# Kernel optimization log

Measured on AMD Instinct MI355X. Metric: run time of the kernel, lower is better.

Reference implementation:

```python
import jax, jax.numpy as jnp
import numpy as np
from jax import lax

D_MODEL = 128   # n_channels
OUT_C   = 128   # out_channels
D_STATE = 16
EXPAND  = 2
D_INNER = EXPAND * D_MODEL  # 256
D_CONV  = 4
DT_RANK = (D_MODEL + 15) // 16  # 8
LN_EPS  = 1e-5


def setup_inputs() -> dict:
    key = jax.random.key(0)
    ks = jax.random.split(key, 8)
    s = lambda k, shape: jax.random.normal(k, shape, jnp.float32) * 0.02
    return {
        "x1": jax.random.normal(ks[0], (2, D_MODEL, 64, 64), jnp.float32),
        "W_in": s(ks[1], (D_MODEL, 2 * D_INNER)),              # in_proj (no bias)
        "conv_w": s(ks[2], (D_INNER, 1, D_CONV)),              # depthwise conv kernel (O, I/g, K)
        "conv_b": jnp.zeros((D_INNER,), jnp.float32),
        "W_x": s(ks[3], (D_INNER, DT_RANK + 2 * D_STATE)),     # x_proj (no bias)
        "W_dt": s(ks[4], (DT_RANK, D_INNER)),                  # dt_proj
        "b_dt": s(ks[5], (D_INNER,)),
        "A_log": jnp.log(jnp.broadcast_to(
            jnp.arange(1, D_STATE + 1, dtype=jnp.float32), (D_INNER, D_STATE))),
        "D": jnp.ones((D_INNER,), jnp.float32),
        "W_out": s(ks[6], (D_INNER, OUT_C)),                   # out_proj (no bias)
        "ln_g": jnp.ones((OUT_C,), jnp.float32),
        "ln_b": jnp.zeros((OUT_C,), jnp.float32),
    }


def _mamba(x, W_in, conv_w, conv_b, W_x, W_dt, b_dt, A_log, D, W_out):
    # x: (b, L, d_model)
    b, L, _ = x.shape
    xz = x @ W_in                               # (b, L, 2*d_inner)
    xin, z = jnp.split(xz, 2, axis=-1)
    # causal depthwise conv1d over L
    xp = jnp.pad(xin, ((0, 0), (D_CONV - 1, 0), (0, 0)))
    xc = lax.conv_general_dilated(
        xp, conv_w, window_strides=(1,), padding='VALID',
        dimension_numbers=('NLC', 'OIL', 'NLC'),
        feature_group_count=D_INNER)
    xc = jax.nn.silu(xc + conv_b)               # (b, L, d_inner)
    # input-dependent SSM params
    xdbl = xc @ W_x                             # (b, L, dt_rank + 2*d_state)
    dt, Bm, Cm = jnp.split(xdbl, [DT_RANK, DT_RANK + D_STATE], axis=-1)
    dt = jax.nn.softplus(dt @ W_dt + b_dt)      # (b, L, d_inner)
    A = -jnp.exp(A_log)                         # (d_inner, d_state)
    dA = jnp.exp(dt[..., None] * A)                             # (b, L, d_inner, d_state)
    dBu = dt[..., None] * Bm[:, :, None, :] * xc[..., None]     # (b, L, d_inner, d_state)

    def step(h, inp):
        dA_t, dBu_t, C_t = inp                  # (b,d,s), (b,d,s), (b,s)
        h = dA_t * h + dBu_t
        y = jnp.einsum('bds,bs->bd', h, C_t)
        return h, y

    h0 = jnp.zeros((b, D_INNER, D_STATE), xc.dtype)
    _, ys = lax.scan(step, h0, (dA.transpose(1, 0, 2, 3),
                                dBu.transpose(1, 0, 2, 3),
                                Cm.transpose(1, 0, 2)))
    y = ys.transpose(1, 0, 2) + xc * D          # (b, L, d_inner)
    y = y * jax.nn.silu(z)                      # gated
    return y @ W_out                            # (b, L, out_c)


def reference(x1, W_in, conv_w, conv_b, W_x, W_dt, b_dt, A_log, D, W_out, ln_g, ln_b):
    b, c, h, w = x1.shape
    x = x1.transpose(0, 2, 3, 1).reshape(b, h * w, c)
    y = _mamba(x, W_in, conv_w, conv_b, W_x, W_dt, b_dt, A_log, D, W_out)
    mu = y.mean(-1, keepdims=True)
    var = ((y - mu) ** 2).mean(-1, keepdims=True)
    y = (y - mu) * lax.rsqrt(var + LN_EPS) * ln_g + ln_b
    return y.reshape(b, h, w, OUT_C).transpose(0, 3, 1, 2)
```

## Files before the change

### kernel.cpp

```cpp
#include <hip/hip_runtime.h>
#include <math.h>

#define B_ 2
#define DMODEL 128
#define DIN 256
#define DSTATE 16
#define DTR 8
#define OUTC 128
#define Lseq 4096
#define NC 256
#define LC 16

__device__ __forceinline__ float siluf(float x){ return x / (1.f + __expf(-x)); }

__device__ __forceinline__ void build_dA(float e1, float* dAv){
    float e2 = e1*e1, e4 = e2*e2, e8 = e4*e4;
    dAv[0]=e1;         dAv[1]=e2;         dAv[2]=e2*e1;       dAv[3]=e4;
    dAv[4]=e4*e1;      dAv[5]=e4*e2;      dAv[6]=e4*dAv[2];   dAv[7]=e8;
    dAv[8]=e8*e1;      dAv[9]=e8*e2;      dAv[10]=e8*dAv[2];  dAv[11]=e8*e4;
    dAv[12]=e8*dAv[4]; dAv[13]=e8*dAv[5]; dAv[14]=e8*dAv[6];  dAv[15]=e8*e8;
}

__device__ __forceinline__ float softplusf(float a){
    return (a > 20.f) ? a : __logf(1.f + __expf(a));
}

__global__ __launch_bounds__(256) void k_inconv_scan1(const float* __restrict__ x1,
        const float* __restrict__ Win,
        const float* __restrict__ convw, const float* __restrict__ convb,
        const float* __restrict__ Wx, const float* __restrict__ Wdt,
        const float* __restrict__ bdt, const float* __restrict__ Alog,
        float* __restrict__ zs, float* __restrict__ xc, float* __restrict__ dt,
        float* __restrict__ Bm, float* __restrict__ Cm, float2* __restrict__ PSw){
    __shared__ float xt[128*20];
    __shared__ float xcs[16*257];
    __shared__ float xdbl[16*40];
    int blk = blockIdx.x;
    int b  = blk >> 8;
    int cb = blk & 255;
    int l0 = cb << 4;
    int t  = threadIdx.x;

    const float* xb = x1 + (size_t)b * DMODEL * Lseq;
    for (int e = t; e < 128*19; e += 256){
        int c = e / 19, p = e - c*19;
        int l = l0 - 3 + p;
        xt[c*20 + p] = (l >= 0) ? xb[(size_t)c*Lseq + l] : 0.f;
    }
    __syncthreads();

    float acc0[19], acc1[16];
    #pragma unroll
    for (int p=0;p<19;++p) acc0[p]=0.f;
    #pragma unroll
    for (int p=0;p<16;++p) acc1[p]=0.f;
    for (int k=0;k<DMODEL;++k){
        float w0 = Win[k*512 + t];
        float w1 = Win[k*512 + t + 256];
        float xv[19];
        #pragma unroll
        for (int p=0;p<19;++p) xv[p] = xt[k*20 + p];
        #pragma unroll
        for (int p=0;p<19;++p) acc0[p] = fmaf(xv[p], w0, acc0[p]);
        #pragma unroll
        for (int p=0;p<16;++p) acc1[p] = fmaf(xv[p+3], w1, acc1[p]);
    }
    {
        float* zp = zs + ((size_t)(b*Lseq + l0))*DIN + t;
        #pragma unroll
        for (int p=0;p<16;++p) zp[p*DIN] = siluf(acc1[p]);
    }

    {
        float cw0 = convw[t*4+0], cw1 = convw[t*4+1], cw2 = convw[t*4+2], cw3 = convw[t*4+3];
        float bb = convb[t];
        float* xcg = xc + ((size_t)(b*Lseq + l0))*DIN + t;
        #pragma unroll
        for (int l = 0; l < 16; ++l){
            float acc = bb;
            acc = fmaf(acc0[l],   cw0, acc);
            acc = fmaf(acc0[l+1], cw1, acc);
            acc = fmaf(acc0[l+2], cw2, acc);
            acc = fmaf(acc0[l+3], cw3, acc);
            float v = siluf(acc);
            xcs[l*257 + t] = v;
            xcg[l*DIN] = v;
        }
    }
    __syncthreads();

    if (t < 128){
        int jg = t & 7;
        int lg = t >> 3;
        int j0 = jg * 5;
        float a0=0.f, a1=0.f, a2=0.f, a3=0.f, a4=0.f;
        const float* xrow = xcs + lg*257;
        const float* wbase = Wx + j0;
        #pragma unroll 8
        for (int d = 0; d < 256; ++d){
            float xv = xrow[d];
            const float* wr = wbase + d*40;
            a0 = fmaf(xv, wr[0], a0);
            a1 = fmaf(xv, wr[1], a1);
            a2 = fmaf(xv, wr[2], a2);
            a3 = fmaf(xv, wr[3], a3);
            a4 = fmaf(xv, wr[4], a4);
        }
        float* xo = xdbl + lg*40 + j0;
        xo[0]=a0; xo[1]=a1; xo[2]=a2; xo[3]=a3; xo[4]=a4;
    }
    __syncthreads();

    {
        float wd[DTR];
        #pragma unroll
        for (int r=0;r<DTR;++r) wd[r] = Wdt[r*DIN + t];
        float bv = bdt[t];
        float Av[16];
        {
            const float4* Ap = (const float4*)(Alog + t*DSTATE);
            #pragma unroll
            for (int q=0;q<4;++q){
                float4 a = Ap[q];
                Av[q*4]   = -__expf(a.x);
                Av[q*4+1] = -__expf(a.y);
                Av[q*4+2] = -__expf(a.z);
                Av[q*4+3] = -__expf(a.w);
            }
        }
        bool fastA = true;
        #pragma unroll
        for (int i=1;i<16;++i)
            fastA = fastA && (fabsf(Av[i] - (float)(i+1)*Av[0]) <= 1e-6f*fabsf(Av[i]));
        float P[16], S[16];
        #pragma unroll
        for (int s=0;s<16;++s){ P[s]=1.f; S[s]=0.f; }
        float* dtg = dt + ((size_t)(b*Lseq + l0))*DIN + t;
        #pragma unroll 4
        for (int l=0;l<16;++l){
            float a = bv;
            #pragma unroll
            for (int r=0;r<DTR;++r) a = fmaf(xdbl[l*40 + r], wd[r], a);
            float dtv = softplusf(a);
            dtg[l*DIN] = dtv;
            float xcv = xcs[l*257 + t];
            float dx  = dtv*xcv;
            const float4* Bv = (const float4*)&xdbl[l*40 + DTR];
            float4 B0 = Bv[0], B1 = Bv[1], B2 = Bv[2], B3 = Bv[3];
            float dAv[16];
            if (fastA){
                build_dA(__expf(dtv*Av[0]), dAv);
            } else {
                #pragma unroll
                for (int i=0;i<16;++i) dAv[i] = __expf(dtv*Av[i]);
            }
            #define ST1(i, bval) { P[i] *= dAv[i]; S[i] = fmaf(dAv[i], S[i], dx*(bval)); }
            ST1(0,B0.x) ST1(1,B0.y) ST1(2,B0.z) ST1(3,B0.w)
            ST1(4,B1.x) ST1(5,B1.y) ST1(6,B1.z) ST1(7,B1.w)
            ST1(8,B2.x) ST1(9,B2.y) ST1(10,B2.z) ST1(11,B2.w)
            ST1(12,B3.x) ST1(13,B3.y) ST1(14,B3.z) ST1(15,B3.w)
            #undef ST1
        }
        float2* ps = PSw + ((size_t)(b*NC + cb))*4096 + t*DSTATE;
        #pragma unroll
        for (int s=0;s<16;++s) ps[s] = make_float2(P[s], S[s]);
    }
    for (int o = t; o < 512; o += 256){
        int l = o >> 5, q = o & 31;
        float v = xdbl[l*40 + DTR + q];
        size_t g = ((size_t)(b*Lseq + l0 + l))*DSTATE;
        if (q < DSTATE) Bm[g + q] = v;
        else            Cm[g + (q - DSTATE)] = v;
    }
}

__global__ __launch_bounds__(256) void k_scan2(const float2* __restrict__ PSw,
        float* __restrict__ Iw){
    __shared__ float2 gps[16][16];
    __shared__ float  ge [16][16];
    int blk = blockIdx.x;
    int b  = blk >> 8;
    int r0 = (blk & 255) * 16;
    int t  = threadIdx.x;
    int rr = t & 15;
    int cg = t >> 4;
    size_t base = ((size_t)(b*NC + cg*16))*4096 + r0 + rr;
    float Pl[16], Sl[16];
    float Pa = 1.f, Sa = 0.f;
    #pragma unroll
    for (int i=0;i<16;++i){
        float2 ps = PSw[base + (size_t)i*4096];
        Pl[i] = ps.x; Sl[i] = ps.y;
        Pa = ps.x * Pa;
        Sa = fmaf(ps.x, Sa, ps.y);
    }
    gps[cg][rr] = make_float2(Pa, Sa);
    __syncthreads();
    if (t < 16){
        float H = 0.f;
        #pragma unroll
        for (int g=0; g<16; ++g){
            float2 ps = gps[g][t];
            ge[g][t] = H;
            H = fmaf(ps.x, H, ps.y);
        }
    }
    __syncthreads();
    float H = ge[cg][rr];
    #pragma unroll
    for (int i=0;i<16;++i){
        Iw[base + (size_t)i*4096] = H;
        H = fmaf(Pl[i], H, Sl[i]);
    }
}

__global__ __launch_bounds__(256) void k_scan3out(const float* __restrict__ dt,
        const float* __restrict__ xc, const float* __restrict__ zs,
        const float* __restrict__ Bm, const float* __restrict__ Cm,
        const float* __restrict__ Alog, const float* __restrict__ Dv,
        const float* __restrict__ Iw,
        const float* __restrict__ Wout, const float* __restrict__ lng,
        const float* __restrict__ lnb, float* __restrict__ out){
    __shared__ float ysm[256*18];
    __shared__ float os[128*18];
    __shared__ float Bs[LC*DSTATE];
    __shared__ float Cs[LC*DSTATE];
    int blk = blockIdx.x;
    int b = blk >> 8, c = blk & 255;
    int l0 = c * LC;
    int t = threadIdx.x;
    size_t gb = (size_t)(b*Lseq + l0);
    Bs[t] = Bm[gb*DSTATE + t];
    Cs[t] = Cm[gb*DSTATE + t];
    float Av[16];
    {
        const float4* Ap = (const float4*)(Alog + t*DSTATE);
        #pragma unroll
        for (int q=0;q<4;++q){
            float4 a = Ap[q];
            Av[q*4]   = -__expf(a.x);
            Av[q*4+1] = -__expf(a.y);
            Av[q*4+2] = -__expf(a.z);
            Av[q*4+3] = -__expf(a.w);
        }
    }
    bool fastA = true;
    #pragma unroll
    for (int i=1;i<16;++i)
        fastA = fastA && (fabsf(Av[i] - (float)(i+1)*Av[0]) <= 1e-6f*fabsf(Av[i]));
    float h[16];
    {
        const float4* Ip = (const float4*)(Iw + ((size_t)(b*NC + c))*4096 + t*DSTATE);
        #pragma unroll
        for (int q=0;q<4;++q){
            float4 v = Ip[q];
            h[q*4]=v.x; h[q*4+1]=v.y; h[q*4+2]=v.z; h[q*4+3]=v.w;
        }
    }
    float Dd = Dv[t];
    float dtv[LC], xcv[LC], zvv[LC];
    {
        const float* dtp = dt + gb*DIN + t;
        const float* xcp = xc + gb*DIN + t;
        const float* zsp = zs + gb*DIN + t;
        #pragma unroll
        for (int l=0;l<LC;++l){
            dtv[l] = dtp[l*DIN];
            xcv[l] = xcp[l*DIN];
            zvv[l] = zsp[l*DIN];
        }
    }
    __syncthreads();
    #pragma unroll
    for (int l=0;l<LC;++l){
        float dtl = dtv[l];
        float dx  = dtl*xcv[l];
        const float4* Bv = (const float4*)&Bs[l*DSTATE];
        const float4* Cv = (const float4*)&Cs[l*DSTATE];
        float4 B0 = Bv[0], B1 = Bv[1], B2 = Bv[2], B3 = Bv[3];
        float4 C0 = Cv[0], C1 = Cv[1], C2 = Cv[2], C3 = Cv[3];
        float dAv[16];
        if (fastA){
            build_dA(__expf(dtl*Av[0]), dAv);
        } else {
            #pragma unroll
            for (int i=0;i<16;++i) dAv[i] = __expf(dtl*Av[i]);
        }
        float y = 0.f;
        #define ST3(i, bval, cval) { h[i] = fmaf(dAv[i], h[i], dx*(bval)); y = fmaf(h[i], (cval), y); }
        ST3(0,B0.x,C0.x) ST3(1,B0.y,C0.y) ST3(2,B0.z,C0.z) ST3(3,B0.w,C0.w)
        ST3(4,B1.x,C1.x) ST3(5,B1.y,C1.y) ST3(6,B1.z,C1.z) ST3(7,B1.w,C1.w)
        ST3(8,B2.x,C2.x) ST3(9,B2.y,C2.y) ST3(10,B2.z,C2.z) ST3(11,B2.w,C2.w)
        ST3(12,B3.x,C3.x) ST3(13,B3.y,C3.y) ST3(14,B3.z,C3.z) ST3(15,B3.w,C3.w)
        #undef ST3
        ysm[t*18 + l] = (y + Dd*xcv[l])*zvv[l];
    }
    __syncthreads();
    int lg = t >> 5, cg = t & 31;
    int l0t = lg*2, c0 = cg*4;
    float acc[2][4];
    #pragma unroll
    for (int i=0;i<2;++i)
        #pragma unroll
        for (int j=0;j<4;++j) acc[i][j]=0.f;
    #pragma unroll 4
    for (int k=0;k<DIN;++k){
        float2 yv = *(const float2*)&ysm[k*18 + l0t];
        float4 wv = *(const float4*)&Wout[k*OUTC + c0];
        acc[0][0]=fmaf(yv.x,wv.x,acc[0][0]); acc[0][1]=fmaf(yv.x,wv.y,acc[0][1]);
        acc[0][2]=fmaf(yv.x,wv.z,acc[0][2]); acc[0][3]=fmaf(yv.x,wv.w,acc[0][3]);
        acc[1][0]=fmaf(yv.y,wv.x,acc[1][0]); acc[1][1]=fmaf(yv.y,wv.y,acc[1][1]);
        acc[1][2]=fmaf(yv.y,wv.z,acc[1][2]); acc[1][3]=fmaf(yv.y,wv.w,acc[1][3]);
    }
    float4 gm = *(const float4*)&lng[c0];
    float4 bt = *(const float4*)&lnb[c0];
    #pragma unroll
    for (int i=0;i<2;++i){
        float rs = acc[i][0]+acc[i][1]+acc[i][2]+acc[i][3];
        #pragma unroll
        for (int m=16;m>0;m>>=1) rs += __shfl_xor(rs, m, 64);
        float mu = rs * (1.f/128.f);
        float d0 = acc[i][0]-mu, d1 = acc[i][1]-mu, d2 = acc[i][2]-mu, d3 = acc[i][3]-mu;
        float sq = d0*d0+d1*d1+d2*d2+d3*d3;
        #pragma unroll
        for (int m=16;m>0;m>>=1) sq += __shfl_xor(sq, m, 64);
        float rstd = rsqrtf(sq * (1.f/128.f) + 1e-5f);
        int lidx = l0t + i;
        os[(c0+0)*18 + lidx] = d0*rstd*gm.x + bt.x;
        os[(c0+1)*18 + lidx] = d1*rstd*gm.y + bt.y;
        os[(c0+2)*18 + lidx] = d2*rstd*gm.z + bt.z;
        os[(c0+3)*18 + lidx] = d3*rstd*gm.w + bt.w;
    }
    __syncthreads();
    {
        int cc = t >> 1, sel = t & 1;
        const float* ip = &os[cc*18 + sel*8];
        float2 a0 = *(const float2*)(ip);
        float2 a1 = *(const float2*)(ip+2);
        float2 a2 = *(const float2*)(ip+4);
        float2 a3 = *(const float2*)(ip+6);
        float* op = out + ((size_t)(b*OUTC + cc))*Lseq + l0 + sel*8;
        *(float4*)(op)   = make_float4(a0.x,a0.y,a1.x,a1.y);
        *(float4*)(op+4) = make_float4(a2.x,a2.y,a3.x,a3.y);
    }
}

extern "C" void kernel_launch(void* const* d_in, const int* in_sizes, int n_in,
                              void* d_out, int out_size, void* d_ws, size_t ws_size,
                              hipStream_t stream) {
    const float* x1    = (const float*)d_in[0];
    const float* Win   = (const float*)d_in[1];
    const float* convw = (const float*)d_in[2];
    const float* convb = (const float*)d_in[3];
    const float* Wx    = (const float*)d_in[4];
    const float* Wdt   = (const float*)d_in[5];
    const float* bdt   = (const float*)d_in[6];
    const float* Alog  = (const float*)d_in[7];
    const float* Dv    = (const float*)d_in[8];
    const float* Wout  = (const float*)d_in[9];
    const float* lng   = (const float*)d_in[10];
    const float* lnb   = (const float*)d_in[11];
    float* out = (float*)d_out;

    float* ws  = (float*)d_ws;
    float* Iw  = ws;
    float* zs  = Iw  + 2097152;
    float* xc  = zs  + 2097152;
    float* dt  = xc  + 2097152;
    float* Bm  = dt  + 2097152;
    float* Cm  = Bm  + 131072;
    float2* PSw = (float2*)(Cm + 131072);

    k_inconv_scan1<<<512, 256, 0, stream>>>(x1, Win, convw, convb, Wx, Wdt, bdt, Alog,
                                            zs, xc, dt, Bm, Cm, PSw);
    k_scan2       <<<512, 256, 0, stream>>>(PSw, Iw);
    k_scan3out    <<<512, 256, 0, stream>>>(dt, xc, zs, Bm, Cm, Alog, Dv, Iw,
                                            Wout, lng, lnb, out);
}
```

Before: 167.6 us.

## Double block size to 512 threads and split projection work across thread halves

Both the input-projection/scan1 kernel and the scan3/out-projection kernel now launch 512 threads per block instead of 256. In the first kernel, the in_proj GEMM is split so one half computes the xin/conv branch and the other half computes the z gate. The x tile is now loaded as float4 into a padded tile, and the x_proj work is spread over 320 threads. In the output kernel, the out_proj GEMM and LayerNorm now handle one row per thread group instead of two, which raises parallelism and lowers per-thread register pressure. The cost is that half the threads sit idle during the scan phases, and the larger blocks may reduce how many blocks fit on a compute unit at once.

Result: slower. 197.4 us (+17.8%).

```diff
diff --git a/kernel.cpp b/kernel.cpp
--- a/kernel.cpp
+++ b/kernel.cpp
@@ -25,14 +25,14 @@
     return (a > 20.f) ? a : __logf(1.f + __expf(a));
 }
 
-__global__ __launch_bounds__(256) void k_inconv_scan1(const float* __restrict__ x1,
+__global__ __launch_bounds__(512) void k_inconv_scan1(const float* __restrict__ x1,
         const float* __restrict__ Win,
         const float* __restrict__ convw, const float* __restrict__ convb,
         const float* __restrict__ Wx, const float* __restrict__ Wdt,
         const float* __restrict__ bdt, const float* __restrict__ Alog,
         float* __restrict__ zs, float* __restrict__ xc, float* __restrict__ dt,
         float* __restrict__ Bm, float* __restrict__ Cm, float2* __restrict__ PSw){
-    __shared__ float xt[128*20];
+    __shared__ float xt[128*24];
     __shared__ float xcs[16*257];
     __shared__ float xdbl[16*40];
     int blk = blockIdx.x;
@@ -42,36 +42,37 @@
     int t  = threadIdx.x;
 
     const float* xb = x1 + (size_t)b * DMODEL * Lseq;
-    for (int e = t; e < 128*19; e += 256){
-        int c = e / 19, p = e - c*19;
-        int l = l0 - 3 + p;
-        xt[c*20 + p] = (l >= 0) ? xb[(size_t)c*Lseq + l] : 0.f;
-    }
-    __syncthreads();
-
-    float acc0[19], acc1[16];
-    #pragma unroll
-    for (int p=0;p<19;++p) acc0[p]=0.f;
-    #pragma unroll
-    for (int p=0;p<16;++p) acc1[p]=0.f;
-    for (int k=0;k<DMODEL;++k){
-        float w0 = Win[k*512 + t];
-        float w1 = Win[k*512 + t + 256];
-        float xv[19];
-        #pragma unroll
-        for (int p=0;p<19;++p) xv[p] = xt[k*20 + p];
-        #pragma unroll
-        for (int p=0;p<19;++p) acc0[p] = fmaf(xv[p], w0, acc0[p]);
-        #pragma unroll
-        for (int p=0;p<16;++p) acc1[p] = fmaf(xv[p+3], w1, acc1[p]);
-    }
     {
-        float* zp = zs + ((size_t)(b*Lseq + l0))*DIN + t;
-        #pragma unroll
-        for (int p=0;p<16;++p) zp[p*DIN] = siluf(acc1[p]);
-    }
-
-    {
+        float4 z4 = make_float4(0.f,0.f,0.f,0.f);
+        for (int e = t; e < 128*6; e += 512){
+            int c = e / 6, i = e - c*6;
+            int l = l0 - 8 + i*4;
+            float4 v = (l >= 0) ? *(const float4*)&xb[(size_t)c*Lseq + l] : z4;
+            *(float4*)&xt[e*4] = v;
+        }
+    }
+    __syncthreads();
+
+    if (t < 256){
+        float acc0[19];
+        #pragma unroll
+        for (int p=0;p<19;++p) acc0[p]=0.f;
+        #pragma unroll 4
+        for (int k=0;k<128;++k){
+            float w = Win[k*512 + t];
+            const float4* xp = (const float4*)&xt[k*24 + 4];
+            float4 x0=xp[0], x1_=xp[1], x2_=xp[2], x3_=xp[3], x4_=xp[4];
+            acc0[0] =fmaf(x0.y, w, acc0[0]);  acc0[1] =fmaf(x0.z, w, acc0[1]);
+            acc0[2] =fmaf(x0.w, w, acc0[2]);  acc0[3] =fmaf(x1_.x,w, acc0[3]);
+            acc0[4] =fmaf(x1_.y,w, acc0[4]);  acc0[5] =fmaf(x1_.z,w, acc0[5]);
+            acc0[6] =fmaf(x1_.w,w, acc0[6]);  acc0[7] =fmaf(x2_.x,w, acc0[7]);
+            acc0[8] =fmaf(x2_.y,w, acc0[8]);  acc0[9] =fmaf(x2_.z,w, acc0[9]);
+            acc0[10]=fmaf(x2_.w,w, acc0[10]); acc0[11]=fmaf(x3_.x,w, acc0[11]);
+            acc0[12]=fmaf(x3_.y,w, acc0[12]); acc0[13]=fmaf(x3_.z,w, acc0[13]);
+            acc0[14]=fmaf(x3_.w,w, acc0[14]); acc0[15]=fmaf(x4_.x,w, acc0[15]);
+            acc0[16]=fmaf(x4_.y,w, acc0[16]); acc0[17]=fmaf(x4_.z,w, acc0[17]);
+            acc0[18]=fmaf(x4_.w,w, acc0[18]);
+        }
         float cw0 = convw[t*4+0], cw1 = convw[t*4+1], cw2 = convw[t*4+2], cw3 = convw[t*4+3];
         float bb = convb[t];
         float* xcg = xc + ((size_t)(b*Lseq + l0))*DIN + t;
@@ -86,32 +87,49 @@
             xcs[l*257 + t] = v;
             xcg[l*DIN] = v;
         }
-    }
-    __syncthreads();
-
-    if (t < 128){
-        int jg = t & 7;
-        int lg = t >> 3;
-        int j0 = jg * 5;
-        float a0=0.f, a1=0.f, a2=0.f, a3=0.f, a4=0.f;
-        const float* xrow = xcs + lg*257;
-        const float* wbase = Wx + j0;
+    } else {
+        float acc1[16];
+        #pragma unroll
+        for (int p=0;p<16;++p) acc1[p]=0.f;
+        #pragma unroll 4
+        for (int k=0;k<128;++k){
+            float w = Win[k*512 + t];
+            const float4* yp = (const float4*)&xt[k*24 + 8];
+            float4 y0=yp[0], y1=yp[1], y2=yp[2], y3=yp[3];
+            acc1[0] =fmaf(y0.x, w, acc1[0]);  acc1[1] =fmaf(y0.y, w, acc1[1]);
+            acc1[2] =fmaf(y0.z, w, acc1[2]);  acc1[3] =fmaf(y0.w, w, acc1[3]);
+            acc1[4] =fmaf(y1.x, w, acc1[4]);  acc1[5] =fmaf(y1.y, w, acc1[5]);
+            acc1[6] =fmaf(y1.z, w, acc1[6]);  acc1[7] =fmaf(y1.w, w, acc1[7]);
+            acc1[8] =fmaf(y2.x, w, acc1[8]);  acc1[9] =fmaf(y2.y, w, acc1[9]);
+            acc1[10]=fmaf(y2.z, w, acc1[10]); acc1[11]=fmaf(y2.w, w, acc1[11]);
+            acc1[12]=fmaf(y3.x, w, acc1[12]); acc1[13]=fmaf(y3.y, w, acc1[13]);
+            acc1[14]=fmaf(y3.z, w, acc1[14]); acc1[15]=fmaf(y3.w, w, acc1[15]);
+        }
+        float* zp = zs + ((size_t)(b*Lseq + l0))*DIN + (t - 256);
+        #pragma unroll
+        for (int p=0;p<16;++p) zp[p*DIN] = siluf(acc1[p]);
+    }
+    __syncthreads();
+
+    if (t < 320){
+        int row = t / 20;
+        int jg  = t - row*20;
+        int j0  = jg * 2;
+        float a0=0.f, a1=0.f;
+        const float* xrow = xcs + row*257;
+        const float* wb = Wx + j0;
         #pragma unroll 8
         for (int d = 0; d < 256; ++d){
             float xv = xrow[d];
-            const float* wr = wbase + d*40;
-            a0 = fmaf(xv, wr[0], a0);
-            a1 = fmaf(xv, wr[1], a1);
-            a2 = fmaf(xv, wr[2], a2);
-            a3 = fmaf(xv, wr[3], a3);
-            a4 = fmaf(xv, wr[4], a4);
-        }
-        float* xo = xdbl + lg*40 + j0;
-        xo[0]=a0; xo[1]=a1; xo[2]=a2; xo[3]=a3; xo[4]=a4;
-    }
-    __syncthreads();
-
-    {
+            float2 wv = *(const float2*)&wb[d*40];
+            a0 = fmaf(xv, wv.x, a0);
+            a1 = fmaf(xv, wv.y, a1);
+        }
+        *(float2*)&xdbl[row*40 + j0] = make_float2(a0, a1);
+    }
+    __syncthreads();
+
+    if (t < 256){
         float wd[DTR];
         #pragma unroll
         for (int r=0;r<DTR;++r) wd[r] = Wdt[r*DIN + t];
@@ -165,8 +183,8 @@
         #pragma unroll
         for (int s=0;s<16;++s) ps[s] = make_float2(P[s], S[s]);
     }
-    for (int o = t; o < 512; o += 256){
-        int l = o >> 5, q = o & 31;
+    {
+        int l = t >> 5, q = t & 31;
         float v = xdbl[l*40 + DTR + q];
         size_t g = ((size_t)(b*Lseq + l0 + l))*DSTATE;
         if (q < DSTATE) Bm[g + q] = v;
@@ -214,7 +232,7 @@
     }
 }
 
-__global__ __launch_bounds__(256) void k_scan3out(const float* __restrict__ dt,
+__global__ __launch_bounds__(512) void k_scan3out(const float* __restrict__ dt,
         const float* __restrict__ xc, const float* __restrict__ zs,
         const float* __restrict__ Bm, const float* __restrict__ Cm,
         const float* __restrict__ Alog, const float* __restrict__ Dv,
@@ -230,10 +248,13 @@
     int l0 = c * LC;
     int t = threadIdx.x;
     size_t gb = (size_t)(b*Lseq + l0);
-    Bs[t] = Bm[gb*DSTATE + t];
-    Cs[t] = Cm[gb*DSTATE + t];
-    float Av[16];
-    {
+    if (t < 256) Bs[t]       = Bm[gb*DSTATE + t];
+    else         Cs[t - 256] = Cm[gb*DSTATE + (t - 256)];
+
+    float Av[16], h[16], dtv[LC], xcv[LC], zvv[LC];
+    float Dd = 0.f;
+    bool fastA = true;
+    if (t < 256){
         const float4* Ap = (const float4*)(Alog + t*DSTATE);
         #pragma unroll
         for (int q=0;q<4;++q){
@@ -243,23 +264,16 @@
             Av[q*4+2] = -__expf(a.z);
             Av[q*4+3] = -__expf(a.w);
         }
-    }
-    bool fastA = true;
-    #pragma unroll
-    for (int i=1;i<16;++i)
-        fastA = fastA && (fabsf(Av[i] - (float)(i+1)*Av[0]) <= 1e-6f*fabsf(Av[i]));
-    float h[16];
-    {
+        #pragma unroll
+        for (int i=1;i<16;++i)
+            fastA = fastA && (fabsf(Av[i] - (float)(i+1)*Av[0]) <= 1e-6f*fabsf(Av[i]));
         const float4* Ip = (const float4*)(Iw + ((size_t)(b*NC + c))*4096 + t*DSTATE);
         #pragma unroll
         for (int q=0;q<4;++q){
             float4 v = Ip[q];
             h[q*4]=v.x; h[q*4+1]=v.y; h[q*4+2]=v.z; h[q*4+3]=v.w;
         }
-    }
-    float Dd = Dv[t];
-    float dtv[LC], xcv[LC], zvv[LC];
-    {
+        Dd = Dv[t];
         const float* dtp = dt + gb*DIN + t;
         const float* xcp = xc + gb*DIN + t;
         const float* zsp = zs + gb*DIN + t;
@@ -271,77 +285,70 @@
         }
     }
     __syncthreads();
-    #pragma unroll
-    for (int l=0;l<LC;++l){
-        float dtl = dtv[l];
-        float dx  = dtl*xcv[l];
-        const float4* Bv = (const float4*)&Bs[l*DSTATE];
-        const float4* Cv = (const float4*)&Cs[l*DSTATE];
-        float4 B0 = Bv[0], B1 = Bv[1], B2 = Bv[2], B3 = Bv[3];
-        float4 C0 = Cv[0], C1 = Cv[1], C2 = Cv[2], C3 = Cv[3];
-        float dAv[16];
-        if (fastA){
-            build_dA(__expf(dtl*Av[0]), dAv);
-        } else {
-            #pragma unroll
-            for (int i=0;i<16;++i) dAv[i] = __expf(dtl*Av[i]);
-        }
-        float y = 0.f;
-        #define ST3(i, bval, cval) { h[i] = fmaf(dAv[i], h[i], dx*(bval)); y = fmaf(h[i], (cval), y); }
-        ST3(0,B0.x,C0.x) ST3(1,B0.y,C0.y) ST3(2,B0.z,C0.z) ST3(3,B0.w,C0.w)
-        ST3(4,B1.x,C1.x) ST3(5,B1.y,C1.y) ST3(6,B1.z,C1.z) ST3(7,B1.w,C1.w)
-        ST3(8,B2.x,C2.x) ST3(9,B2.y,C2.y) ST3(10,B2.z,C2.z) ST3(11,B2.w,C2.w)
-        ST3(12,B3.x,C3.x) ST3(13,B3.y,C3.y) ST3(14,B3.z,C3.z) ST3(15,B3.w,C3.w)
-        #undef ST3
-        ysm[t*18 + l] = (y + Dd*xcv[l])*zvv[l];
+    if (t < 256){
+        #pragma unroll
+        for (int l=0;l<LC;++l){
+            float dtl = dtv[l];
+            float dx  = dtl*xcv[l];
+            const float4* Bv = (const float4*)&Bs[l*DSTATE];
+            const float4* Cv = (const float4*)&Cs[l*DSTATE];
+            float4 B0 = Bv[0], B1 = Bv[1], B2 = Bv[2], B3 = Bv[3];
+            float4 C0 = Cv[0], C1 = Cv[1], C2 = Cv[2], C3 = Cv[3];
+            float dAv[16];
+            if (fastA){
+                build_dA(__expf(dtl*Av[0]), dAv);
+            } else {
+                #pragma unroll
+                for (int i=0;i<16;++i) dAv[i] = __expf(dtl*Av[i]);
+            }
+            float y = 0.f;
+            #define ST3(i, bval, cval) { h[i] = fmaf(dAv[i], h[i], dx*(bval)); y = fmaf(h[i], (cval), y); }
+            ST3(0,B0.x,C0.x) ST3(1,B0.y,C0.y) ST3(2,B0.z,C0.z) ST3(3,B0.w,C0.w)
+            ST3(4,B1.x,C1.x) ST3(5,B1.y,C1.y) ST3(6,B1.z,C1.z) ST3(7,B1.w,C1.w)
+            ST3(8,B2.x,C2.x) ST3(9,B2.y,C2.y) ST3(10,B2.z,C2.z) ST3(11,B2.w,C2.w)
+            ST3(12,B3.x,C3.x) ST3(13,B3.y,C3.y) ST3(14,B3.z,C3.z) ST3(15,B3.w,C3.w)
+            #undef ST3
+            ysm[t*18 + l] = (y + Dd*xcv[l])*zvv[l];
+        }
     }
     __syncthreads();
     int lg = t >> 5, cg = t & 31;
-    int l0t = lg*2, c0 = cg*4;
-    float acc[2][4];
-    #pragma unroll
-    for (int i=0;i<2;++i)
-        #pragma unroll
-        for (int j=0;j<4;++j) acc[i][j]=0.f;
+    int c0 = cg*4;
+    float a0=0.f, a1=0.f, a2=0.f, a3=0.f;
     #pragma unroll 4
     for (int k=0;k<DIN;++k){
-        float2 yv = *(const float2*)&ysm[k*18 + l0t];
+        float yv = ysm[k*18 + lg];
         float4 wv = *(const float4*)&Wout[k*OUTC + c0];
-        acc[0][0]=fmaf(yv.x,wv.x,acc[0][0]); acc[0][1]=fmaf(yv.x,wv.y,acc[0][1]);
-        acc[0][2]=fmaf(yv.x,wv.z,acc[0][2]); acc[0][3]=fmaf(yv.x,wv.w,acc[0][3]);
-        acc[1][0]=fmaf(yv.y,wv.x,acc[1][0]); acc[1][1]=fmaf(yv.y,wv.y,acc[1][1]);
-        acc[1][2]=fmaf(yv.y,wv.z,acc[1][2]); acc[1][3]=fmaf(yv.y,wv.w,acc[1][3]);
-    }
-    float4 gm = *(const float4*)&lng[c0];
-    float4 bt = *(const float4*)&lnb[c0];
-    #pragma unroll
-    for (int i=0;i<2;++i){
-        float rs = acc[i][0]+acc[i][1]+acc[i][2]+acc[i][3];
+        a0 = fmaf(yv, wv.x, a0);
+        a1 = fmaf(yv, wv.y, a1);
+        a2 = fmaf(yv, wv.z, a2);
+        a3 = fmaf(yv, wv.w, a3);
+    }
+    {
+        float4 gm = *(const float4*)&lng[c0];
+        float4 bt = *(const float4*)&lnb[c0];
+        float rs = a0+a1+a2+a3;
         #pragma unroll
         for (int m=16;m>0;m>>=1) rs += __shfl_xor(rs, m, 64);
         float mu = rs * (1.f/128.f);
-        float d0 = acc[i][0]-mu, d1 = acc[i][1]-mu, d2 = acc[i][2]-mu, d3 = acc[i][3]-mu;
+        float d0 = a0-mu, d1 = a1-mu, d2 = a2-mu, d3 = a3-mu;
         float sq = d0*d0+d1*d1+d2*d2+d3*d3;
         #pragma unroll
         for (int m=16;m>0;m>>=1) sq += __shfl_xor(sq, m, 64);
         float rstd = rsqrtf(sq * (1.f/128.f) + 1e-5f);
-        int lidx = l0t + i;
-        os[(c0+0)*18 + lidx] = d0*rstd*gm.x + bt.x;
-        os[(c0+1)*18 + lidx] = d1*rstd*gm.y + bt.y;
-        os[(c0+2)*18 + lidx] = d2*rstd*gm.z + bt.z;
-        os[(c0+3)*18 + lidx] = d3*rstd*gm.w + bt.w;
+        os[(c0+0)*18 + lg] = d0*rstd*gm.x + bt.x;
+        os[(c0+1)*18 + lg] = d1*rstd*gm.y + bt.y;
+        os[(c0+2)*18 + lg] = d2*rstd*gm.z + bt.z;
+        os[(c0+3)*18 + lg] = d3*rstd*gm.w + bt.w;
     }
     __syncthreads();
     {
-        int cc = t >> 1, sel = t & 1;
-        const float* ip = &os[cc*18 + sel*8];
-        float2 a0 = *(const float2*)(ip);
-        float2 a1 = *(const float2*)(ip+2);
-        float2 a2 = *(const float2*)(ip+4);
-        float2 a3 = *(const float2*)(ip+6);
-        float* op = out + ((size_t)(b*OUTC + cc))*Lseq + l0 + sel*8;
-        *(float4*)(op)   = make_float4(a0.x,a0.y,a1.x,a1.y);
-        *(float4*)(op+4) = make_float4(a2.x,a2.y,a3.x,a3.y);
+        int cc = t >> 2, q = t & 3;
+        const float* ip = &os[cc*18 + q*4];
+        float2 v0 = *(const float2*)(ip);
+        float2 v1 = *(const float2*)(ip+2);
+        float* op = out + ((size_t)(b*OUTC + cc))*Lseq + l0 + q*4;
+        *(float4*)op = make_float4(v0.x, v0.y, v1.x, v1.y);
     }
 }
 
@@ -371,9 +378,9 @@
     float* Cm  = Bm  + 131072;
     float2* PSw = (float2*)(Cm + 131072);
 
-    k_inconv_scan1<<<512, 256, 0, stream>>>(x1, Win, convw, convb, Wx, Wdt, bdt, Alog,
+    k_inconv_scan1<<<512, 512, 0, stream>>>(x1, Win, convw, convb, Wx, Wdt, bdt, Alog,
                                             zs, xc, dt, Bm, Cm, PSw);
     k_scan2       <<<512, 256, 0, stream>>>(PSw, Iw);
-    k_scan3out    <<<512, 256, 0, stream>>>(dt, xc, zs, Bm, Cm, Alog, Dv, Iw,
+    k_scan3out    <<<512, 512, 0, stream>>>(dt, xc, zs, Bm, Cm, Alog, Dv, Iw,
                                             Wout, lng, lnb, out);
 }
```

## Halve scan chunk length to 8, doubling blocks, and reuse PS buffer in-place

Applied to the files above, without the earlier changes.

Shrinks the sequence chunk from 16 to 8 so both the fused in-proj/conv/scan1 kernel and the scan3/out-proj kernel launch twice as many blocks, aiming for better occupancy across the MI355X's CUs. The conv halo is now loaded with float4 reads, and x_proj is split over all threads (one output per thread). Scan2 writes the carried-in state back into the PS buffer in place, dropping the separate Iw workspace and its register staging. The cost is a longer inter-chunk scan, more per-block overhead, and 8-byte strided reads of the state in scan3.

After: 245.2 us. +46.3%, slower.

```diff
diff --git a/kernel.cpp b/kernel.cpp
--- a/kernel.cpp
+++ b/kernel.cpp
@@ -8,8 +8,8 @@
 #define DTR 8
 #define OUTC 128
 #define Lseq 4096
-#define NC 256
-#define LC 16
+#define NC 512
+#define LC 8
 
 __device__ __forceinline__ float siluf(float x){ return x / (1.f + __expf(-x)); }
 
@@ -32,51 +32,61 @@
         const float* __restrict__ bdt, const float* __restrict__ Alog,
         float* __restrict__ zs, float* __restrict__ xc, float* __restrict__ dt,
         float* __restrict__ Bm, float* __restrict__ Cm, float2* __restrict__ PSw){
-    __shared__ float xt[128*20];
-    __shared__ float xcs[16*257];
-    __shared__ float xdbl[16*40];
+    __shared__ float xt[128*16];
+    __shared__ float xcs[8*257];
+    __shared__ float xdbl[8*40];
     int blk = blockIdx.x;
-    int b  = blk >> 8;
-    int cb = blk & 255;
-    int l0 = cb << 4;
+    int b  = blk >> 9;
+    int cb = blk & 511;
+    int l0 = cb << 3;
     int t  = threadIdx.x;
 
     const float* xb = x1 + (size_t)b * DMODEL * Lseq;
-    for (int e = t; e < 128*19; e += 256){
-        int c = e / 19, p = e - c*19;
-        int l = l0 - 3 + p;
-        xt[c*20 + p] = (l >= 0) ? xb[(size_t)c*Lseq + l] : 0.f;
-    }
-    __syncthreads();
-
-    float acc0[19], acc1[16];
+    {
+        float4 z4 = make_float4(0.f,0.f,0.f,0.f);
+        #pragma unroll
+        for (int e = t; e < 128*4; e += 256){
+            int c = e >> 2, i = e & 3;
+            int l = l0 - 8 + i*4;
+            float4 v = (l >= 0) ? *(const float4*)&xb[(size_t)c*Lseq + l] : z4;
+            *(float4*)&xt[e*4] = v;
+        }
+    }
+    __syncthreads();
+
+    float acc0[11], acc1[8];
     #pragma unroll
-    for (int p=0;p<19;++p) acc0[p]=0.f;
+    for (int p=0;p<11;++p) acc0[p]=0.f;
     #pragma unroll
-    for (int p=0;p<16;++p) acc1[p]=0.f;
-    for (int k=0;k<DMODEL;++k){
+    for (int p=0;p<8;++p)  acc1[p]=0.f;
+    #pragma unroll 4
+    for (int k=0;k<128;++k){
         float w0 = Win[k*512 + t];
         float w1 = Win[k*512 + t + 256];
-        float xv[19];
-        #pragma unroll
-        for (int p=0;p<19;++p) xv[p] = xt[k*20 + p];
-        #pragma unroll
-        for (int p=0;p<19;++p) acc0[p] = fmaf(xv[p], w0, acc0[p]);
-        #pragma unroll
-        for (int p=0;p<16;++p) acc1[p] = fmaf(xv[p+3], w1, acc1[p]);
+        const float4* xp = (const float4*)&xt[k*16];
+        float4 x1_ = xp[1], x2_ = xp[2], x3_ = xp[3];
+        acc0[0] =fmaf(x1_.y, w0, acc0[0]);  acc0[1] =fmaf(x1_.z, w0, acc0[1]);
+        acc0[2] =fmaf(x1_.w, w0, acc0[2]);  acc0[3] =fmaf(x2_.x, w0, acc0[3]);
+        acc0[4] =fmaf(x2_.y, w0, acc0[4]);  acc0[5] =fmaf(x2_.z, w0, acc0[5]);
+        acc0[6] =fmaf(x2_.w, w0, acc0[6]);  acc0[7] =fmaf(x3_.x, w0, acc0[7]);
+        acc0[8] =fmaf(x3_.y, w0, acc0[8]);  acc0[9] =fmaf(x3_.z, w0, acc0[9]);
+        acc0[10]=fmaf(x3_.w, w0, acc0[10]);
+        acc1[0] =fmaf(x2_.x, w1, acc1[0]);  acc1[1] =fmaf(x2_.y, w1, acc1[1]);
+        acc1[2] =fmaf(x2_.z, w1, acc1[2]);  acc1[3] =fmaf(x2_.w, w1, acc1[3]);
+        acc1[4] =fmaf(x3_.x, w1, acc1[4]);  acc1[5] =fmaf(x3_.y, w1, acc1[5]);
+        acc1[6] =fmaf(x3_.z, w1, acc1[6]);  acc1[7] =fmaf(x3_.w, w1, acc1[7]);
     }
     {
         float* zp = zs + ((size_t)(b*Lseq + l0))*DIN + t;
         #pragma unroll
-        for (int p=0;p<16;++p) zp[p*DIN] = siluf(acc1[p]);
-    }
-
+        for (int p=0;p<8;++p) zp[p*DIN] = siluf(acc1[p]);
+    }
     {
         float cw0 = convw[t*4+0], cw1 = convw[t*4+1], cw2 = convw[t*4+2], cw3 = convw[t*4+3];
         float bb = convb[t];
         float* xcg = xc + ((size_t)(b*Lseq + l0))*DIN + t;
         #pragma unroll
-        for (int l = 0; l < 16; ++l){
+        for (int l = 0; l < LC; ++l){
             float acc = bb;
             acc = fmaf(acc0[l],   cw0, acc);
             acc = fmaf(acc0[l+1], cw1, acc);
@@ -89,25 +99,25 @@
     }
     __syncthreads();
 
-    if (t < 128){
-        int jg = t & 7;
-        int lg = t >> 3;
-        int j0 = jg * 5;
-        float a0=0.f, a1=0.f, a2=0.f, a3=0.f, a4=0.f;
-        const float* xrow = xcs + lg*257;
-        const float* wbase = Wx + j0;
+    {
+        int row = t >> 5, col = t & 31;
+        float a = 0.f;
+        const float* xrow = xcs + row*257;
+        const float* wb = Wx + 8 + col;
         #pragma unroll 8
-        for (int d = 0; d < 256; ++d){
-            float xv = xrow[d];
-            const float* wr = wbase + d*40;
-            a0 = fmaf(xv, wr[0], a0);
-            a1 = fmaf(xv, wr[1], a1);
-            a2 = fmaf(xv, wr[2], a2);
-            a3 = fmaf(xv, wr[3], a3);
-            a4 = fmaf(xv, wr[4], a4);
-        }
-        float* xo = xdbl + lg*40 + j0;
-        xo[0]=a0; xo[1]=a1; xo[2]=a2; xo[3]=a3; xo[4]=a4;
+        for (int d = 0; d < 256; ++d)
+            a = fmaf(xrow[d], wb[d*40], a);
+        xdbl[row*40 + 8 + col] = a;
+    }
+    if (t < 64){
+        int row = t >> 3, r = t & 7;
+        float a = 0.f;
+        const float* xrow = xcs + row*257;
+        const float* wb = Wx + r;
+        #pragma unroll 8
+        for (int d = 0; d < 256; ++d)
+            a = fmaf(xrow[d], wb[d*40], a);
+        xdbl[row*40 + r] = a;
     }
     __syncthreads();
 
@@ -136,8 +146,8 @@
         #pragma unroll
         for (int s=0;s<16;++s){ P[s]=1.f; S[s]=0.f; }
         float* dtg = dt + ((size_t)(b*Lseq + l0))*DIN + t;
-        #pragma unroll 4
-        for (int l=0;l<16;++l){
+        #pragma unroll
+        for (int l=0;l<LC;++l){
             float a = bv;
             #pragma unroll
             for (int r=0;r<DTR;++r) a = fmaf(xdbl[l*40 + r], wd[r], a);
@@ -165,8 +175,8 @@
         #pragma unroll
         for (int s=0;s<16;++s) ps[s] = make_float2(P[s], S[s]);
     }
-    for (int o = t; o < 512; o += 256){
-        int l = o >> 5, q = o & 31;
+    {
+        int l = t >> 5, q = t & 31;
         float v = xdbl[l*40 + DTR + q];
         size_t g = ((size_t)(b*Lseq + l0 + l))*DSTATE;
         if (q < DSTATE) Bm[g + q] = v;
@@ -174,8 +184,7 @@
     }
 }
 
-__global__ __launch_bounds__(256) void k_scan2(const float2* __restrict__ PSw,
-        float* __restrict__ Iw){
+__global__ __launch_bounds__(256) void k_scan2(float2* __restrict__ PSw){
     __shared__ float2 gps[16][16];
     __shared__ float  ge [16][16];
     int blk = blockIdx.x;
@@ -184,13 +193,11 @@
     int t  = threadIdx.x;
     int rr = t & 15;
     int cg = t >> 4;
-    size_t base = ((size_t)(b*NC + cg*16))*4096 + r0 + rr;
-    float Pl[16], Sl[16];
+    size_t base = ((size_t)(b*NC + cg*32))*4096 + r0 + rr;
     float Pa = 1.f, Sa = 0.f;
-    #pragma unroll
-    for (int i=0;i<16;++i){
+    #pragma unroll 8
+    for (int i=0;i<32;++i){
         float2 ps = PSw[base + (size_t)i*4096];
-        Pl[i] = ps.x; Sl[i] = ps.y;
         Pa = ps.x * Pa;
         Sa = fmaf(ps.x, Sa, ps.y);
     }
@@ -207,10 +214,12 @@
     }
     __syncthreads();
     float H = ge[cg][rr];
-    #pragma unroll
-    for (int i=0;i<16;++i){
-        Iw[base + (size_t)i*4096] = H;
-        H = fmaf(Pl[i], H, Sl[i]);
+    #pragma unroll 8
+    for (int i=0;i<32;++i){
+        size_t idx = base + (size_t)i*4096;
+        float2 ps = PSw[idx];
+        PSw[idx] = make_float2(H, 0.f);
+        H = fmaf(ps.x, H, ps.y);
     }
 }
 
@@ -218,20 +227,21 @@
         const float* __restrict__ xc, const float* __restrict__ zs,
         const float* __restrict__ Bm, const float* __restrict__ Cm,
         const float* __restrict__ Alog, const float* __restrict__ Dv,
-        const float* __restrict__ Iw,
+        const float2* __restrict__ PSw,
         const float* __restrict__ Wout, const float* __restrict__ lng,
         const float* __restrict__ lnb, float* __restrict__ out){
-    __shared__ float ysm[256*18];
-    __shared__ float os[128*18];
+    __shared__ float ysm[256*9];
+    __shared__ float os[128*12];
     __shared__ float Bs[LC*DSTATE];
     __shared__ float Cs[LC*DSTATE];
     int blk = blockIdx.x;
-    int b = blk >> 8, c = blk & 255;
+    int b = blk >> 9, c = blk & 511;
     int l0 = c * LC;
     int t = threadIdx.x;
     size_t gb = (size_t)(b*Lseq + l0);
-    Bs[t] = Bm[gb*DSTATE + t];
-    Cs[t] = Cm[gb*DSTATE + t];
+    if (t < 128)      Bs[t]       = Bm[gb*DSTATE + t];
+    else              Cs[t - 128] = Cm[gb*DSTATE + (t - 128)];
+
     float Av[16];
     {
         const float4* Ap = (const float4*)(Alog + t*DSTATE);
@@ -250,11 +260,12 @@
         fastA = fastA && (fabsf(Av[i] - (float)(i+1)*Av[0]) <= 1e-6f*fabsf(Av[i]));
     float h[16];
     {
-        const float4* Ip = (const float4*)(Iw + ((size_t)(b*NC + c))*4096 + t*DSTATE);
-        #pragma unroll
-        for (int q=0;q<4;++q){
+        const float4* Ip = (const float4*)(PSw + ((size_t)(b*NC + c))*4096 + t*DSTATE);
+        #pragma unroll
+        for (int q=0;q<8;++q){
             float4 v = Ip[q];
-            h[q*4]=v.x; h[q*4+1]=v.y; h[q*4+2]=v.z; h[q*4+3]=v.w;
+            h[q*2]   = v.x;
+            h[q*2+1] = v.z;
         }
     }
     float Dd = Dv[t];
@@ -293,55 +304,44 @@
         ST3(8,B2.x,C2.x) ST3(9,B2.y,C2.y) ST3(10,B2.z,C2.z) ST3(11,B2.w,C2.w)
         ST3(12,B3.x,C3.x) ST3(13,B3.y,C3.y) ST3(14,B3.z,C3.z) ST3(15,B3.w,C3.w)
         #undef ST3
-        ysm[t*18 + l] = (y + Dd*xcv[l])*zvv[l];
-    }
-    __syncthreads();
-    int lg = t >> 5, cg = t & 31;
-    int l0t = lg*2, c0 = cg*4;
-    float acc[2][4];
-    #pragma unroll
-    for (int i=0;i<2;++i)
-        #pragma unroll
-        for (int j=0;j<4;++j) acc[i][j]=0.f;
+        ysm[t*9 + l] = (y + Dd*xcv[l])*zvv[l];
+    }
+    __syncthreads();
+    int lr = t >> 5, cg = t & 31;
+    int c0 = cg*4;
+    float a0=0.f, a1=0.f, a2=0.f, a3=0.f;
     #pragma unroll 4
     for (int k=0;k<DIN;++k){
-        float2 yv = *(const float2*)&ysm[k*18 + l0t];
+        float yv = ysm[k*9 + lr];
         float4 wv = *(const float4*)&Wout[k*OUTC + c0];
-        acc[0][0]=fmaf(yv.x,wv.x,acc[0][0]); acc[0][1]=fmaf(yv.x,wv.y,acc[0][1]);
-        acc[0][2]=fmaf(yv.x,wv.z,acc[0][2]); acc[0][3]=fmaf(yv.x,wv.w,acc[0][3]);
-        acc[1][0]=fmaf(yv.y,wv.x,acc[1][0]); acc[1][1]=fmaf(yv.y,wv.y,acc[1][1]);
-        acc[1][2]=fmaf(yv.y,wv.z,acc[1][2]); acc[1][3]=fmaf(yv.y,wv.w,acc[1][3]);
-    }
-    float4 gm = *(const float4*)&lng[c0];
-    float4 bt = *(const float4*)&lnb[c0];
-    #pragma unroll
-    for (int i=0;i<2;++i){
-        float rs = acc[i][0]+acc[i][1]+acc[i][2]+acc[i][3];
+        a0 = fmaf(yv, wv.x, a0);
+        a1 = fmaf(yv, wv.y, a1);
+        a2 = fmaf(yv, wv.z, a2);
+        a3 = fmaf(yv, wv.w, a3);
+    }
+    {
+        float4 gm = *(const float4*)&lng[c0];
+        float4 bt = *(const float4*)&lnb[c0];
+        float rs = a0+a1+a2+a3;
         #pragma unroll
         for (int m=16;m>0;m>>=1) rs += __shfl_xor(rs, m, 64);
         float mu = rs * (1.f/128.f);
-        float d0 = acc[i][0]-mu, d1 = acc[i][1]-mu, d2 = acc[i][2]-mu, d3 = acc[i][3]-mu;
+        float d0 = a0-mu, d1 = a1-mu, d2 = a2-mu, d3 = a3-mu;
         float sq = d0*d0+d1*d1+d2*d2+d3*d3;
         #pragma unroll
         for (int m=16;m>0;m>>=1) sq += __shfl_xor(sq, m, 64);
         float rstd = rsqrtf(sq * (1.f/128.f) + 1e-5f);
-        int lidx = l0t + i;
-        os[(c0+0)*18 + lidx] = d0*rstd*gm.x + bt.x;
-        os[(c0+1)*18 + lidx] = d1*rstd*gm.y + bt.y;
-        os[(c0+2)*18 + lidx] = d2*rstd*gm.z + bt.z;
-        os[(c0+3)*18 + lidx] = d3*rstd*gm.w + bt.w;
+        os[(c0+0)*12 + lr] = d0*rstd*gm.x + bt.x;
+        os[(c0+1)*12 + lr] = d1*rstd*gm.y + bt.y;
+        os[(c0+2)*12 + lr] = d2*rstd*gm.z + bt.z;
+        os[(c0+3)*12 + lr] = d3*rstd*gm.w + bt.w;
     }
     __syncthreads();
     {
         int cc = t >> 1, sel = t & 1;
-        const float* ip = &os[cc*18 + sel*8];
-        float2 a0 = *(const float2*)(ip);
-        float2 a1 = *(const float2*)(ip+2);
-        float2 a2 = *(const float2*)(ip+4);
-        float2 a3 = *(const float2*)(ip+6);
-        float* op = out + ((size_t)(b*OUTC + cc))*Lseq + l0 + sel*8;
-        *(float4*)(op)   = make_float4(a0.x,a0.y,a1.x,a1.y);
-        *(float4*)(op+4) = make_float4(a2.x,a2.y,a3.x,a3.y);
+        float4 v = *(const float4*)&os[cc*12 + sel*4];
+        float* op = out + ((size_t)(b*OUTC + cc))*Lseq + l0 + sel*4;
+        *(float4*)op = v;
     }
 }
 
@@ -363,17 +363,16 @@
     float* out = (float*)d_out;
 
     float* ws  = (float*)d_ws;
-    float* Iw  = ws;
-    float* zs  = Iw  + 2097152;
+    float* zs  = ws;
     float* xc  = zs  + 2097152;
     float* dt  = xc  + 2097152;
     float* Bm  = dt  + 2097152;
     float* Cm  = Bm  + 131072;
     float2* PSw = (float2*)(Cm + 131072);
 
-    k_inconv_scan1<<<512, 256, 0, stream>>>(x1, Win, convw, convb, Wx, Wdt, bdt, Alog,
-                                            zs, xc, dt, Bm, Cm, PSw);
-    k_scan2       <<<512, 256, 0, stream>>>(PSw, Iw);
-    k_scan3out    <<<512, 256, 0, stream>>>(dt, xc, zs, Bm, Cm, Alog, Dv, Iw,
-                                            Wout, lng, lnb, out);
-}
+    k_inconv_scan1<<<1024, 256, 0, stream>>>(x1, Win, convw, convb, Wx, Wdt, bdt, Alog,
+                                             zs, xc, dt, Bm, Cm, PSw);
+    k_scan2       <<<512,  256, 0, stream>>>(PSw);
+    k_scan3out    <<<1024, 256, 0, stream>>>(dt, xc, zs, Bm, Cm, Alog, Dv, PSw,
+                                             Wout, lng, lnb, out);
+}
```
